# Kernel tuning notes

Hardware: AMD Instinct MI355X
Metric: run time of the kernel (lower is better)

Reference implementation:

```python
import jax, jax.numpy as jnp
import numpy as np

B, SP, SS = 8, 512, 64          # batch, prefix seq len, suffix seq len
HP, HS = 2048, 1024             # prefix / suffix hidden sizes
NH, NKV, HD = 8, 1, 256         # heads, kv heads, head dim (GQA groups = 8)
IP, IS = 16384, 4096            # MLP intermediate sizes
COND = 1024                     # adaRMSNorm conditioning dim
T = SP + SS
EPS = 1e-6
SCALE = HD ** -0.5
ROPE_BASE = 10000.0


def _rms(x):
    var = jnp.mean(jnp.square(x), axis=-1, keepdims=True)
    return x * jax.lax.rsqrt(var + EPS)


def _rot_half(x):
    x1, x2 = jnp.split(x, 2, axis=-1)
    return jnp.concatenate([-x2, x1], axis=-1)


def setup_inputs() -> dict:
    key = jax.random.key(0)
    ks = iter(jax.random.split(key, 40))
    rn = lambda shape, s=0.02: jax.random.normal(next(ks), shape, dtype=jnp.float32) * s
    return dict(
        x_prefix=rn((B, SP, HP), 1.0),
        x_suffix=rn((B, SS, HS), 1.0),
        cond=rn((B, COND), 1.0),
        attention_mask=jnp.zeros((B, 1, T, T), jnp.float32),
        p_ln1_w=rn((HP,)),
        p_q=rn((NH * HD, HP)), p_k=rn((NKV * HD, HP)), p_v=rn((NKV * HD, HP)), p_o=rn((HP, NH * HD)),
        p_ln2_w=rn((HP,)),
        p_gate=rn((IP, HP)), p_up=rn((IP, HP)), p_down=rn((HP, IP)),
        s_ada1_w=rn((3 * HS, COND)), s_ada1_b=rn((3 * HS,)),
        s_q=rn((NH * HD, HS)), s_k=rn((NKV * HD, HS)), s_v=rn((NKV * HD, HS)), s_o=rn((HS, NH * HD)),
        s_ada2_w=rn((3 * HS, COND)), s_ada2_b=rn((3 * HS,)),
        s_gate=rn((IS, HS)), s_up=rn((IS, HS)), s_down=rn((HS, IS)),
        position_ids=jnp.broadcast_to(jnp.arange(T, dtype=jnp.int32), (B, T)),
    )


def _ada_norm(x, cond, w, b):
    # AdaRMSNormV2: rms(x)*(1+scale)+shift; gate returned separately
    mod = cond @ w.T + b                      # [B, 3*HS]
    scale, shift, gate = jnp.split(mod, 3, axis=-1)
    normed = _rms(x) * (1.0 + scale[:, None, :]) + shift[:, None, :]
    return normed, gate[:, None, :]


def _qkv(h, wq, wk, wv):
    b, t, _ = h.shape
    q = (h @ wq.T).reshape(b, t, NH, HD).transpose(0, 2, 1, 3)   # [B,NH,t,HD]
    k = (h @ wk.T).reshape(b, t, NKV, HD).transpose(0, 2, 1, 3)  # [B,1,t,HD]
    v = (h @ wv.T).reshape(b, t, NKV, HD).transpose(0, 2, 1, 3)
    return q, k, v


def reference(x_prefix, x_suffix, cond, attention_mask,
              p_ln1_w, p_q, p_k, p_v, p_o, p_ln2_w, p_gate, p_up, p_down,
              s_ada1_w, s_ada1_b, s_q, s_k, s_v, s_o, s_ada2_w, s_ada2_b,
              s_gate, s_up, s_down, position_ids):
    # --- pre-attention norms ---
    hp = _rms(x_prefix) * (1.0 + p_ln1_w)                  # plain RMSNorm, gate=None
    hs, gate1 = _ada_norm(x_suffix, cond, s_ada1_w, s_ada1_b)

    qp, kp, vp = _qkv(hp, p_q, p_k, p_v)
    qs, ks, vs = _qkv(hs, s_q, s_k, s_v)
    q = jnp.concatenate([qp, qs], axis=2)                  # [B,NH,T,HD]
    k = jnp.concatenate([kp, ks], axis=2)                  # [B,1,T,HD]
    v = jnp.concatenate([vp, vs], axis=2)

    # --- RoPE over joint sequence ---
    inv_freq = 1.0 / (ROPE_BASE ** (jnp.arange(0, HD, 2, dtype=jnp.float32) / HD))
    freqs = position_ids.astype(jnp.float32)[:, :, None] * inv_freq  # [B,T,HD/2]
    emb = jnp.concatenate([freqs, freqs], axis=-1)
    cos = jnp.cos(emb)[:, None]                            # [B,1,T,HD]
    sin = jnp.sin(emb)[:, None]
    q = q * cos + _rot_half(q) * sin
    k = k * cos + _rot_half(k) * sin

    # --- joint attention (GQA: single kv head broadcast over NH query heads) ---
    k0, v0 = k[:, 0], v[:, 0]                              # [B,T,HD]
    scores = jnp.einsum('bhqd,bkd->bhqk', q, k0) * SCALE
    scores = scores + attention_mask
    probs = jax.nn.softmax(scores, axis=-1)
    attn = jnp.einsum('bhqk,bkd->bhqd', probs, v0)
    attn = attn.transpose(0, 2, 1, 3).reshape(B, T, NH * HD)

    a_p, a_s = attn[:, :SP], attn[:, SP:]

    # --- prefix stream: o_proj + residual + RMSNorm + GeGLU MLP ---
    res_p = x_prefix + a_p @ p_o.T
    h = _rms(res_p) * (1.0 + p_ln2_w)
    mlp_p = (jax.nn.gelu(h @ p_gate.T, approximate=True) * (h @ p_up.T)) @ p_down.T
    out_prefix = res_p + mlp_p

    # --- suffix stream: gated residual + adaRMSNorm + GeGLU MLP + gated residual ---
    res_s = x_suffix + (a_s @ s_o.T) * gate1
    h2, gate2 = _ada_norm(res_s, cond, s_ada2_w, s_ada2_b)
    mlp_s = (jax.nn.gelu(h2 @ s_gate.T, approximate=True) * (h2 @ s_up.T)) @ s_down.T
    out_suffix = res_s + mlp_s * gate2

    return (out_prefix, out_suffix)
```

## Files before the change

### kernel.cpp

```cpp
#include <hip/hip_runtime.h>
#include <cstdint>
#include <cstddef>

typedef __bf16 bf;
typedef __attribute__((ext_vector_type(8))) __bf16 bf16x8;
typedef __attribute__((ext_vector_type(4))) float f32x4;
typedef long long ll;

#define DEV __device__ __forceinline__

constexpr int Tt = 576;
constexpr int NHh = 8;
constexpr float EPSf = 1e-6f;
constexpr float SCALEf = 0.0625f;
constexpr float LN1E4_OVER_128 = 0.07195578515606394f;

constexpr int EPI_F32 = 0, EPI_SCALE_BF16 = 1, EPI_BF16 = 2, EPI_GELU_BF16 = 3,
              EPI_MUL_BF16 = 4, EPI_RES_F32 = 5, EPI_RESGATE_F32 = 6;

DEV float wsum(float v) {
#pragma unroll
  for (int o = 32; o > 0; o >>= 1) v += __shfl_xor(v, o, 64);
  return v;
}
DEV float wmaxr(float v) {
#pragma unroll
  for (int o = 32; o > 0; o >>= 1) v = fmaxf(v, __shfl_xor(v, o, 64));
  return v;
}
DEV float gelu_tanh(float x) {
  float x3 = x * x * x;
  float t = tanhf(0.7978845608028654f * (x + 0.044715f * x3));
  return 0.5f * x * (1.0f + t);
}

DEV void gld16(const void* g, void* l) {
  __builtin_amdgcn_global_load_lds(
      (__attribute__((address_space(1))) void*)(g),
      (__attribute__((address_space(3))) void*)(l), 16, 0, 0);
}


__global__ void f2b_k(const float* __restrict__ s, bf* __restrict__ d, int n8) {
  int i = blockIdx.x * 256 + threadIdx.x;
  int stride = gridDim.x * 256;
  for (; i < n8; i += stride) {
    f32x4 a = ((const f32x4*)s)[i * 2];
    f32x4 b = ((const f32x4*)s)[i * 2 + 1];
    bf16x8 w;
    w[0] = (bf)a[0]; w[1] = (bf)a[1]; w[2] = (bf)a[2]; w[3] = (bf)a[3];
    w[4] = (bf)b[0]; w[5] = (bf)b[1]; w[6] = (bf)b[2]; w[7] = (bf)b[3];
    ((bf16x8*)d)[i] = w;
  }
}

__global__ void rms_scale_2048(const float* __restrict__ x, const float* __restrict__ w,
                               bf* __restrict__ out) {
  int row = blockIdx.x;
  int tid = threadIdx.x;
  const float* xr = x + (ll)row * 2048;
  f32x4 a = *(const f32x4*)(xr + tid * 4);
  f32x4 b = *(const f32x4*)(xr + 1024 + tid * 4);
  float ss = a[0]*a[0]+a[1]*a[1]+a[2]*a[2]+a[3]*a[3]
           + b[0]*b[0]+b[1]*b[1]+b[2]*b[2]+b[3]*b[3];
  ss = wsum(ss);
  __shared__ float red[4];
  if ((tid & 63) == 0) red[tid >> 6] = ss;
  __syncthreads();
  float tot = red[0] + red[1] + red[2] + red[3];
  float sc = rsqrtf(tot * (1.0f / 2048.0f) + EPSf);
  bf* o = out + (ll)row * 2048;
#pragma unroll
  for (int j = 0; j < 4; j++) {
    int c0 = tid * 4 + j;
    o[c0]        = (bf)(a[j] * sc * (1.0f + w[c0]));
    o[1024 + c0] = (bf)(b[j] * sc * (1.0f + w[1024 + c0]));
  }
}

__global__ void ada_mod_k(const float* __restrict__ cond, const float* __restrict__ w,
                          const float* __restrict__ bias, float* __restrict__ mod) {
  int n = blockIdx.x * 256 + threadIdx.x;
  int b = blockIdx.y;
  const float* c = cond + b * 1024;
  const float* wr = w + (ll)n * 1024;
  float s = 0.f;
  for (int k = 0; k < 1024; k += 4) {
    f32x4 cv = *(const f32x4*)(c + k);
    f32x4 wv = *(const f32x4*)(wr + k);
    s += cv[0]*wv[0] + cv[1]*wv[1] + cv[2]*wv[2] + cv[3]*wv[3];
  }
  mod[b * 3072 + n] = s + bias[n];
}

__global__ void ada_norm_k(const float* __restrict__ x, const float* __restrict__ mod,
                           bf* __restrict__ out) {
  int row = blockIdx.x;
  int b = row >> 6;
  int tid = threadIdx.x;
  const float* xr = x + (ll)row * 1024;
  f32x4 a = *(const f32x4*)(xr + tid * 4);
  float ss = a[0]*a[0] + a[1]*a[1] + a[2]*a[2] + a[3]*a[3];
  ss = wsum(ss);
  __shared__ float red[4];
  if ((tid & 63) == 0) red[tid >> 6] = ss;
  __syncthreads();
  float tot = red[0] + red[1] + red[2] + red[3];
  float sc = rsqrtf(tot * (1.0f / 1024.0f) + EPSf);
  const float* m = mod + b * 3072;
  bf* o = out + (ll)row * 1024;
#pragma unroll
  for (int j = 0; j < 4; j++) {
    int c = tid * 4 + j;
    o[c] = (bf)(a[j] * sc * (1.0f + m[c]) + m[1024 + c]);
  }
}

__global__ void rope_k(const float* __restrict__ qkv,
                       const int* __restrict__ pos, bf* __restrict__ qb,
                       bf* __restrict__ kb, bf* __restrict__ vT) {
  int bt = blockIdx.x;
  int b = bt / Tt, t = bt - b * Tt;
  int tid = threadIdx.x;
  float p = (float)pos[bt];
  const float* qr = qkv + (ll)bt * 2560;
#pragma unroll
  for (int j = 0; j < 4; j++) {
    int pi = tid + 256 * j;
    int h = pi >> 7, d = pi & 127;
    float ang = p * expf((float)d * (-LN1E4_OVER_128));
    float sn = sinf(ang), cs = cosf(ang);
    float x1 = qr[h * 256 + d], x2 = qr[h * 256 + d + 128];
    bf* qo = qb + ((ll)(b * NHh + h) * Tt + t) * 256;
    qo[d]       = (bf)(x1 * cs - x2 * sn);
    qo[d + 128] = (bf)(x2 * cs + x1 * sn);
  }
  const float* kvr = qr + 2048;
  if (tid < 128) {
    int d = tid;
    float ang = p * expf((float)d * (-LN1E4_OVER_128));
    float sn = sinf(ang), cs = cosf(ang);
    float x1 = kvr[d], x2 = kvr[d + 128];
    bf* ko = kb + (ll)bt * 256;
    ko[d]       = (bf)(x1 * cs - x2 * sn);
    ko[d + 128] = (bf)(x2 * cs + x1 * sn);
  } else {
    int d = tid - 128;
    const float* vv = kvr + 256;
    vT[((ll)b * 256 + d) * Tt + t]       = (bf)vv[d];
    vT[((ll)b * 256 + d + 128) * Tt + t] = (bf)vv[d + 128];
  }
}

__global__ void softmax_k(const bf* __restrict__ scores, const float* __restrict__ mask,
                          bf* __restrict__ probs) {
  int rowg = blockIdx.x * 4 + (threadIdx.x >> 6);
  int lane = threadIdx.x & 63;
  int z = rowg / Tt;
  int t = rowg - z * Tt;
  int b = z >> 3;
  const bf* s = scores + (ll)rowg * Tt;
  const float* mr = mask + ((ll)b * Tt + t) * Tt;
  float v[9];
#pragma unroll
  for (int j = 0; j < 9; j++) {
    int c = lane + j * 64;
    v[j] = (float)s[c] + mr[c];
  }
  float mx = v[0];
#pragma unroll
  for (int j = 1; j < 9; j++) mx = fmaxf(mx, v[j]);
  mx = wmaxr(mx);
  float sum = 0.f;
#pragma unroll
  for (int j = 0; j < 9; j++) { v[j] = __expf(v[j] - mx); sum += v[j]; }
  sum = wsum(sum);
  float inv = 1.0f / sum;
  bf* pr = probs + (ll)rowg * Tt;
#pragma unroll
  for (int j = 0; j < 9; j++) pr[lane + j * 64] = (bf)(v[j] * inv);
}


struct GemmArgs {
  const bf* A; ll sA; int lda;
  const void* Bp; ll sB; int ldb; int zdivB;
  void* C; ll sC; ll sC2; int zdivC; int ldc;
  int M, N, K;
  const float* res; ll sRes;
  const float* gate; ll sGate;
  const bf* aux; ll sAux;
  float alpha;
};

template <int EPI>
DEV void epilogue(const GemmArgs& g, f32x4 (&acc)[4][4], int z, int m0, int n0,
                  int lane, int wr, int wc) {
  const ll coff = (ll)(z / g.zdivC) * g.sC + (ll)(z % g.zdivC) * g.sC2;
  const int r0 = (lane >> 4) * 4;
  const int cc = lane & 15;
#pragma unroll
  for (int m = 0; m < 4; m++) {
#pragma unroll
    for (int n = 0; n < 4; n++) {
      int col = n0 + wc * 64 + n * 16 + cc;
      if (col >= g.N) continue;
#pragma unroll
      for (int r = 0; r < 4; r++) {
        int row = m0 + wr * 64 + m * 16 + r0 + r;
        if (row >= g.M) continue;
        float v = acc[m][n][r];
        ll idx = (ll)row * g.ldc + col;
        if constexpr (EPI == EPI_F32) {
          ((float*)g.C)[coff + idx] = v;
        } else if constexpr (EPI == EPI_SCALE_BF16) {
          ((bf*)g.C)[coff + idx] = (bf)(v * g.alpha);
        } else if constexpr (EPI == EPI_BF16) {
          ((bf*)g.C)[coff + idx] = (bf)v;
        } else if constexpr (EPI == EPI_GELU_BF16) {
          ((bf*)g.C)[coff + idx] = (bf)gelu_tanh(v);
        } else if constexpr (EPI == EPI_MUL_BF16) {
          float a0 = (float)g.aux[(ll)z * g.sAux + idx];
          ((bf*)g.C)[coff + idx] = (bf)(a0 * v);
        } else if constexpr (EPI == EPI_RES_F32) {
          ((float*)g.C)[coff + idx] = g.res[(ll)z * g.sRes + idx] + v;
        } else if constexpr (EPI == EPI_RESGATE_F32) {
          ((float*)g.C)[coff + idx] =
              g.res[(ll)z * g.sRes + idx] + v * g.gate[(ll)z * g.sGate + col];
        }
      }
    }
  }
}

template <int EPI, int BN>
__global__ __launch_bounds__(512) void gemm_8p(GemmArgs g) {
  constexpr int NF = BN / 64;
  constexpr int WN = BN / 4;
  const int z = blockIdx.z;
  const int m0 = blockIdx.x * 256;
  const int n0 = blockIdx.y * BN;
  const int tid = threadIdx.x;
  const int lane = tid & 63;
  const int wv = tid >> 6;
  const int wr = wv >> 2;
  const int wc = wv & 3;

  const bf* A = g.A + (ll)z * g.sA;
  const bf* B = (const bf*)g.Bp + (ll)(z / g.zdivB) * g.sB;

  __shared__ __align__(16) bf lA[2][256 * 64];
  __shared__ __align__(16) bf lB[2][BN * 64];

  f32x4 acc[8][NF];
  f32x4 zero = {0.f, 0.f, 0.f, 0.f};
#pragma unroll
  for (int m = 0; m < 8; m++)
#pragma unroll
    for (int n = 0; n < NF; n++) acc[m][n] = zero;

  const int lrow = lane >> 3;
  const int lsrc = ((lane & 7) ^ lrow) * 8;

  auto stage128 = [&](const bf* src, int ld, int grow0, bf* lds) {
#pragma unroll
    for (int i = 0; i < 2; i++) {
      int chunk = wv * 2 + i;
      gld16(src + (ll)(grow0 + chunk * 8 + lrow) * ld + lsrc, lds + chunk * 512);
    }
  };

  const int NT = g.K >> 6;
  stage128(B, g.ldb, n0, &lB[0][0]);
  if (BN == 256) stage128(B, g.ldb, n0 + 128, &lB[0][128 * 64]);
  stage128(A, g.lda, m0, &lA[0][0]);
  stage128(A, g.lda, m0 + 128, &lA[0][128 * 64]);
  asm volatile("s_waitcnt vmcnt(0)" ::: "memory");
  __builtin_amdgcn_s_barrier();

  for (int t = 0; t < NT; ++t) {
    const int c = t & 1;
    const int nx = (t + 1 < NT) ? t + 1 : t;
    const ll kkn = (ll)nx * 64;
    bf16x8 bv[NF][2];
#pragma unroll
    for (int p = 0; p < 4; ++p) {
      if (p == 0) {
#pragma unroll
        for (int n = 0; n < NF; ++n)
#pragma unroll
          for (int kb = 0; kb < 2; ++kb) {
            int row = wc * WN + n * 16 + (lane & 15);
            int ko = kb * 32 + (lane >> 4) * 8;
            bv[n][kb] = *(const bf16x8*)&lB[c][row * 64 + (ko ^ ((row & 7) * 8))];
          }
      }
      bf16x8 af[2][2];
#pragma unroll
      for (int ml = 0; ml < 2; ++ml)
#pragma unroll
        for (int kb = 0; kb < 2; ++kb) {
          int row = wr * 128 + (2 * p + ml) * 16 + (lane & 15);
          int ko = kb * 32 + (lane >> 4) * 8;
          af[ml][kb] = *(const bf16x8*)&lA[c][row * 64 + (ko ^ ((row & 7) * 8))];
        }
      if (p == 0) {
        stage128(B + kkn, g.ldb, n0, &lB[1 - c][0]);
        if (BN == 256) stage128(B + kkn, g.ldb, n0 + 128, &lB[1 - c][128 * 64]);
      } else if (p == 1) {
        stage128(A + kkn, g.lda, m0, &lA[1 - c][0]);
        stage128(A + kkn, g.lda, m0 + 128, &lA[1 - c][128 * 64]);
      }
      __builtin_amdgcn_s_barrier();
      asm volatile("s_waitcnt lgkmcnt(0)" ::: "memory");
      __builtin_amdgcn_s_setprio(1);
#pragma unroll
      for (int kb = 0; kb < 2; ++kb)
#pragma unroll
        for (int ml = 0; ml < 2; ++ml)
#pragma unroll
          for (int n = 0; n < NF; ++n)
            acc[2 * p + ml][n] = __builtin_amdgcn_mfma_f32_16x16x32_bf16(
                af[ml][kb], bv[n][kb], acc[2 * p + ml][n], 0, 0, 0);
      __builtin_amdgcn_s_setprio(0);
      if (p == 3) asm volatile("s_waitcnt vmcnt(0)" ::: "memory");
      __builtin_amdgcn_s_barrier();
    }
  }

  const ll coff = (ll)(z / g.zdivC) * g.sC + (ll)(z % g.zdivC) * g.sC2;
  const int r0 = (lane >> 4) * 4;
  const int cc = lane & 15;
#pragma unroll
  for (int m = 0; m < 8; m++) {
#pragma unroll
    for (int n = 0; n < NF; n++) {
      int col = n0 + wc * WN + n * 16 + cc;
#pragma unroll
      for (int r = 0; r < 4; r++) {
        int row = m0 + wr * 128 + m * 16 + r0 + r;
        float v = acc[m][n][r];
        ll idx = (ll)row * g.ldc + col;
        if constexpr (EPI == EPI_F32) {
          ((float*)g.C)[coff + idx] = v;
        } else if constexpr (EPI == EPI_GELU_BF16) {
          ((bf*)g.C)[coff + idx] = (bf)gelu_tanh(v);
        } else if constexpr (EPI == EPI_MUL_BF16) {
          float a0 = (float)g.aux[(ll)z * g.sAux + idx];
          ((bf*)g.C)[coff + idx] = (bf)(a0 * v);
        } else if constexpr (EPI == EPI_RES_F32) {
          ((float*)g.C)[coff + idx] = g.res[(ll)z * g.sRes + idx] + v;
        }
      }
    }
  }
}

struct FusedArgs {
  const bf* A; int lda;
  const bf* B1; const bf* B2; int ldb;
  bf* C; int ldc;
  int K;
};

__global__ __launch_bounds__(512) void gemm_8pf(FusedArgs g) {
  const int m0 = blockIdx.x * 256;
  const int n0 = blockIdx.y * 128;
  const int tid = threadIdx.x;
  const int lane = tid & 63;
  const int wv = tid >> 6;
  const int wr = wv >> 2;
  const int wc = wv & 3;

  __shared__ __align__(16) bf lA[2][256 * 64];
  __shared__ __align__(16) bf lB1[2][128 * 64];
  __shared__ __align__(16) bf lB2[2][128 * 64];

  f32x4 acc1[8][2], acc2[8][2];
  f32x4 zero = {0.f, 0.f, 0.f, 0.f};
#pragma unroll
  for (int m = 0; m < 8; m++)
#pragma unroll
    for (int n = 0; n < 2; n++) { acc1[m][n] = zero; acc2[m][n] = zero; }

  const int lrow = lane >> 3;
  const int lsrc = ((lane & 7) ^ lrow) * 8;

  auto stage128 = [&](const bf* src, int ld, int grow0, bf* lds) {
#pragma unroll
    for (int i = 0; i < 2; i++) {
      int chunk = wv * 2 + i;
      gld16(src + (ll)(grow0 + chunk * 8 + lrow) * ld + lsrc, lds + chunk * 512);
    }
  };

  const int NT = g.K >> 6;
  stage128(g.B1, g.ldb, n0, &lB1[0][0]);
  stage128(g.B2, g.ldb, n0, &lB2[0][0]);
  stage128(g.A, g.lda, m0, &lA[0][0]);
  stage128(g.A, g.lda, m0 + 128, &lA[0][128 * 64]);
  asm volatile("s_waitcnt vmcnt(0)" ::: "memory");
  __builtin_amdgcn_s_barrier();

  for (int t = 0; t < NT; ++t) {
    const int c = t & 1;
    const int nx = (t + 1 < NT) ? t + 1 : t;
    const ll kkn = (ll)nx * 64;
    bf16x8 b1v[2][2], b2v[2][2];
#pragma unroll
    for (int p = 0; p < 4; ++p) {
      if (p == 0) {
#pragma unroll
        for (int n = 0; n < 2; ++n)
#pragma unroll
          for (int kb = 0; kb < 2; ++kb) {
            int row = wc * 32 + n * 16 + (lane & 15);
            int ko = kb * 32 + (lane >> 4) * 8;
            int sw = row * 64 + (ko ^ ((row & 7) * 8));
            b1v[n][kb] = *(const bf16x8*)&lB1[c][sw];
            b2v[n][kb] = *(const bf16x8*)&lB2[c][sw];
          }
      }
      bf16x8 af[2][2];
#pragma unroll
      for (int ml = 0; ml < 2; ++ml)
#pragma unroll
        for (int kb = 0; kb < 2; ++kb) {
          int row = wr * 128 + (2 * p + ml) * 16 + (lane & 15);
          int ko = kb * 32 + (lane >> 4) * 8;
          af[ml][kb] = *(const bf16x8*)&lA[c][row * 64 + (ko ^ ((row & 7) * 8))];
        }
      if (p == 0) {
        stage128(g.B1 + kkn, g.ldb, n0, &lB1[1 - c][0]);
        stage128(g.B2 + kkn, g.ldb, n0, &lB2[1 - c][0]);
      } else if (p == 1) {
        stage128(g.A + kkn, g.lda, m0, &lA[1 - c][0]);
        stage128(g.A + kkn, g.lda, m0 + 128, &lA[1 - c][128 * 64]);
      }
      __builtin_amdgcn_s_barrier();
      asm volatile("s_waitcnt lgkmcnt(0)" ::: "memory");
      __builtin_amdgcn_s_setprio(1);
#pragma unroll
      for (int kb = 0; kb < 2; ++kb)
#pragma unroll
        for (int ml = 0; ml < 2; ++ml)
#pragma unroll
          for (int n = 0; n < 2; ++n) {
            acc1[2 * p + ml][n] = __builtin_amdgcn_mfma_f32_16x16x32_bf16(
                af[ml][kb], b1v[n][kb], acc1[2 * p + ml][n], 0, 0, 0);
            acc2[2 * p + ml][n] = __builtin_amdgcn_mfma_f32_16x16x32_bf16(
                af[ml][kb], b2v[n][kb], acc2[2 * p + ml][n], 0, 0, 0);
          }
      __builtin_amdgcn_s_setprio(0);
      if (p == 3) asm volatile("s_waitcnt vmcnt(0)" ::: "memory");
      __builtin_amdgcn_s_barrier();
    }
  }

  const int r0 = (lane >> 4) * 4;
  const int cc = lane & 15;
#pragma unroll
  for (int m = 0; m < 8; m++) {
#pragma unroll
    for (int n = 0; n < 2; n++) {
      int col = n0 + wc * 32 + n * 16 + cc;
#pragma unroll
      for (int r = 0; r < 4; r++) {
        int row = m0 + wr * 128 + m * 16 + r0 + r;
        g.C[(ll)row * g.ldc + col] =
            (bf)(gelu_tanh(acc1[m][n][r]) * acc2[m][n][r]);
      }
    }
  }
}

template <int EPI>
__global__ __launch_bounds__(256) void gemm_p(GemmArgs g) {
  const int z = blockIdx.z;
  const int m0 = blockIdx.x * 128;
  const int n0 = blockIdx.y * 128;
  const int tid = threadIdx.x;
  const int lane = tid & 63;
  const int wid = tid >> 6;
  const int wr = wid >> 1, wc = wid & 1;

  const bf* A = g.A + (ll)z * g.sA;
  const bf* B = (const bf*)g.Bp + (ll)(z / g.zdivB) * g.sB;

  __shared__ __align__(16) bf lA[2][128 * 64];
  __shared__ __align__(16) bf lB[2][128 * 64];

  f32x4 acc[4][4];
  f32x4 zero = {0.f, 0.f, 0.f, 0.f};
#pragma unroll
  for (int m = 0; m < 4; m++)
#pragma unroll
    for (int n = 0; n < 4; n++) acc[m][n] = zero;

  const int lrow = lane >> 3;
  const int lsrc = ((lane & 7) ^ lrow) * 8;

  auto stage = [&](int kt, int bsel) {
    const ll kk = (ll)kt * 64;
#pragma unroll
    for (int i = 0; i < 4; i++) {
      int rr = wid * 32 + i * 8;
      int ra = m0 + rr + lrow; if (ra > g.M - 1) ra = g.M - 1;
      gld16(A + (ll)ra * g.lda + kk + lsrc, &lA[bsel][rr * 64]);
      int rb = n0 + rr + lrow; if (rb > g.N - 1) rb = g.N - 1;
      gld16(B + (ll)rb * g.ldb + kk + lsrc, &lB[bsel][rr * 64]);
    }
  };

  const int nt = g.K >> 6;
  stage(0, 0);
  stage(nt > 1 ? 1 : 0, 1);

  for (int t = 0; t < nt; ++t) {
    const int cur = t & 1;
    asm volatile("s_waitcnt vmcnt(8)" ::: "memory");
    __builtin_amdgcn_s_barrier();
    asm volatile("" ::: "memory");
#pragma unroll
    for (int kb = 0; kb < 2; kb++) {
      const int ko = kb * 32 + (lane >> 4) * 8;
      bf16x8 af[4], bv[4];
#pragma unroll
      for (int m = 0; m < 4; m++) {
        int row = wr * 64 + m * 16 + (lane & 15);
        af[m] = *(const bf16x8*)&lA[cur][row * 64 + (ko ^ ((row & 7) * 8))];
      }
#pragma unroll
      for (int n = 0; n < 4; n++) {
        int row = wc * 64 + n * 16 + (lane & 15);
        bv[n] = *(const bf16x8*)&lB[cur][row * 64 + (ko ^ ((row & 7) * 8))];
      }
      __builtin_amdgcn_s_setprio(1);
#pragma unroll
      for (int m = 0; m < 4; m++)
#pragma unroll
        for (int n = 0; n < 4; n++)
          acc[m][n] = __builtin_amdgcn_mfma_f32_16x16x32_bf16(af[m], bv[n], acc[m][n], 0, 0, 0);
      __builtin_amdgcn_s_setprio(0);
    }
    asm volatile("" ::: "memory");
    __builtin_amdgcn_s_barrier();
    asm volatile("" ::: "memory");
    int nxt = t + 2; if (nxt > nt - 1) nxt = nt - 1;
    stage(nxt, cur);
  }
  epilogue<EPI>(g, acc, z, m0, n0, lane, wr, wc);
}

template <int EPI>
__global__ __launch_bounds__(256) void gemm_rs(GemmArgs g) {
  const int z = blockIdx.z;
  const int m0 = blockIdx.x * 128;
  const int n0 = blockIdx.y * 128;
  const int tid = threadIdx.x;
  const int lane = tid & 63;
  const int wid = tid >> 6;
  const int wr = wid >> 1, wc = wid & 1;

  const bf* A = g.A + (ll)z * g.sA;
  const float* Bf = (const float*)g.Bp + (ll)(z / g.zdivB) * g.sB;

  __shared__ __align__(16) bf lA[128 * 64];
  __shared__ __align__(16) bf lB[128 * 64];

  f32x4 acc[4][4];
  f32x4 zero = {0.f, 0.f, 0.f, 0.f};
#pragma unroll
  for (int m = 0; m < 4; m++)
#pragma unroll
    for (int n = 0; n < 4; n++) acc[m][n] = zero;

  const int srow = tid >> 3;
  const int scol = (tid & 7) * 8;

  for (int kk = 0; kk < g.K; kk += 64) {
#pragma unroll
    for (int i = 0; i < 4; i++) {
      int r = m0 + i * 32 + srow;
      if (r > g.M - 1) r = g.M - 1;
      f32x4 v = *(const f32x4*)(A + (ll)r * g.lda + kk + scol);
      *(f32x4*)&lA[(i * 32 + srow) * 64 + scol] = v;
    }
#pragma unroll
    for (int i = 0; i < 4; i++) {
      int r = n0 + i * 32 + srow;
      if (r > g.N - 1) r = g.N - 1;
      const float* src = Bf + (ll)r * g.ldb + kk + scol;
      f32x4 v0 = *(const f32x4*)(src);
      f32x4 v1 = *(const f32x4*)(src + 4);
      bf16x8 w;
      w[0] = (bf)v0[0]; w[1] = (bf)v0[1]; w[2] = (bf)v0[2]; w[3] = (bf)v0[3];
      w[4] = (bf)v1[0]; w[5] = (bf)v1[1]; w[6] = (bf)v1[2]; w[7] = (bf)v1[3];
      *(bf16x8*)&lB[(i * 32 + srow) * 64 + scol] = w;
    }
    __syncthreads();
#pragma unroll
    for (int kb = 0; kb < 2; kb++) {
      const int ko = kb * 32 + (lane >> 4) * 8;
      bf16x8 af[4], bfv[4];
#pragma unroll
      for (int m = 0; m < 4; m++)
        af[m] = *(const bf16x8*)&lA[(wr * 64 + m * 16 + (lane & 15)) * 64 + ko];
#pragma unroll
      for (int n = 0; n < 4; n++)
        bfv[n] = *(const bf16x8*)&lB[(wc * 64 + n * 16 + (lane & 15)) * 64 + ko];
#pragma unroll
      for (int m = 0; m < 4; m++)
#pragma unroll
        for (int n = 0; n < 4; n++)
          acc[m][n] = __builtin_amdgcn_mfma_f32_16x16x32_bf16(af[m], bfv[n], acc[m][n], 0, 0, 0);
    }
    __syncthreads();
  }
  epilogue<EPI>(g, acc, z, m0, n0, lane, wr, wc);
}


static GemmArgs mkG(const bf* A, ll sA, int lda, const void* Bp, ll sB, int ldb, int zdivB,
                    void* C, ll sC, ll sC2, int zdivC, int ldc, int M, int N, int K) {
  GemmArgs g{};
  g.A = A; g.sA = sA; g.lda = lda;
  g.Bp = Bp; g.sB = sB; g.ldb = ldb; g.zdivB = zdivB;
  g.C = C; g.sC = sC; g.sC2 = sC2; g.zdivC = zdivC; g.ldc = ldc;
  g.M = M; g.N = N; g.K = K;
  g.res = nullptr; g.sRes = 0; g.gate = nullptr; g.sGate = 0; g.aux = nullptr; g.sAux = 0;
  g.alpha = 1.0f;
  return g;
}

extern "C" void kernel_launch(void* const* d_in, const int* in_sizes, int n_in,
                              void* d_out, int out_size, void* d_ws, size_t ws_size,
                              hipStream_t stream) {
  (void)in_sizes; (void)n_in; (void)out_size;
  const float* x_prefix = (const float*)d_in[0];
  const float* x_suffix = (const float*)d_in[1];
  const float* cond     = (const float*)d_in[2];
  const float* mask     = (const float*)d_in[3];
  const float* p_ln1_w  = (const float*)d_in[4];
  const float* p_q      = (const float*)d_in[5];
  const float* p_k      = (const float*)d_in[6];
  const float* p_v      = (const float*)d_in[7];
  const float* p_o      = (const float*)d_in[8];
  const float* p_ln2_w  = (const float*)d_in[9];
  const float* p_gate   = (const float*)d_in[10];
  const float* p_up     = (const float*)d_in[11];
  const float* p_down   = (const float*)d_in[12];
  const float* s_ada1_w = (const float*)d_in[13];
  const float* s_ada1_b = (const float*)d_in[14];
  const float* s_q      = (const float*)d_in[15];
  const float* s_k      = (const float*)d_in[16];
  const float* s_v      = (const float*)d_in[17];
  const float* s_o      = (const float*)d_in[18];
  const float* s_ada2_w = (const float*)d_in[19];
  const float* s_ada2_b = (const float*)d_in[20];
  const float* s_gate   = (const float*)d_in[21];
  const float* s_up     = (const float*)d_in[22];
  const float* s_down   = (const float*)d_in[23];
  const int*   pos      = (const int*)d_in[24];

  char* base = (char*)d_ws;
  size_t off = 0;
  auto alloc = [&](size_t bytes) {
    char* p = base + off;
    off = (off + bytes + 255) & ~(size_t)255;
    return p;
  };
  float* qkv   = (float*)alloc(8ll * Tt * 2560 * 4);
  bf* hp     = (bf*)alloc(4096ll * 2048 * 2);
  bf* hs     = (bf*)alloc(512ll * 1024 * 2);
  float* mod1 = (float*)alloc(8 * 3072 * 4);
  float* mod2 = (float*)alloc(8 * 3072 * 4);
  bf* qb     = (bf*)alloc(64ll * Tt * 256 * 2);
  bf* kb     = (bf*)alloc(8ll * Tt * 256 * 2);
  bf* vT     = (bf*)alloc(8ll * 256 * Tt * 2);
  bf* scores = (bf*)alloc(64ll * Tt * Tt * 2);
  float* res_p = (float*)alloc(8ll * 512 * 2048 * 4);
  float* res_s = (float*)alloc(8ll * 64 * 1024 * 4);
  bf* gbuf   = (bf*)alloc(4096ll * 16384 * 2);

  bf* attn   = (bf*)qkv;
  bf* hbuf   = hp;
  bf* h2     = hs;
  bf* probs  = scores;
  bf* gbuf_s = gbuf;

  struct WEnt { const float* src; bf* dst; ll n; };
  WEnt went[14] = {
    {p_q,    nullptr, 2048ll * 2048}, {p_k,    nullptr, 256ll * 2048},
    {p_v,    nullptr, 256ll * 2048},  {p_o,    nullptr, 2048ll * 2048},
    {p_gate, nullptr, 16384ll * 2048},{p_up,   nullptr, 16384ll * 2048},
    {p_down, nullptr, 2048ll * 16384},{s_q,    nullptr, 2048ll * 1024},
    {s_k,    nullptr, 256ll * 1024},  {s_v,    nullptr, 256ll * 1024},
    {s_o,    nullptr, 1024ll * 2048}, {s_gate, nullptr, 4096ll * 1024},
    {s_up,   nullptr, 4096ll * 1024}, {s_down, nullptr, 1024ll * 4096},
  };
  for (int i = 0; i < 14; i++) went[i].dst = (bf*)alloc((size_t)went[i].n * 2);
  const bool conv = (off <= ws_size);

  float* outp = (float*)d_out;
  float* outs = outp + 8ll * 512 * 2048;

  dim3 blk(256);

  if (conv) {
    for (int i = 0; i < 14; i++) {
      int n8 = (int)(went[i].n / 8);
      int grid = (n8 + 255) / 256; if (grid > 4096) grid = 4096;
      f2b_k<<<grid, 256, 0, stream>>>(went[i].src, went[i].dst, n8);
    }
  }
  const bf* w_pqkv = went[0].dst;
  const bf* w_po = went[3].dst, *w_pg = went[4].dst, *w_pu = went[5].dst,
          *w_pd = went[6].dst;
  const bf* w_sqkv = went[7].dst;
  const bf* w_so = went[10].dst, *w_sg = went[11].dst,
          *w_su = went[12].dst, *w_sd = went[13].dst;

  auto launchW = [&](int epi, GemmArgs g, const float* wf32, const bf* wbf,
                     dim3 grid) {
    if (conv) {
      g.Bp = wbf;
      switch (epi) {
        case EPI_F32:        gemm_p<EPI_F32><<<grid, blk, 0, stream>>>(g); break;
        case EPI_GELU_BF16:  gemm_p<EPI_GELU_BF16><<<grid, blk, 0, stream>>>(g); break;
        case EPI_MUL_BF16:   gemm_p<EPI_MUL_BF16><<<grid, blk, 0, stream>>>(g); break;
        case EPI_RES_F32:    gemm_p<EPI_RES_F32><<<grid, blk, 0, stream>>>(g); break;
        case EPI_RESGATE_F32:gemm_p<EPI_RESGATE_F32><<<grid, blk, 0, stream>>>(g); break;
      }
    } else {
      g.Bp = wf32;
      switch (epi) {
        case EPI_F32:        gemm_rs<EPI_F32><<<grid, blk, 0, stream>>>(g); break;
        case EPI_GELU_BF16:  gemm_rs<EPI_GELU_BF16><<<grid, blk, 0, stream>>>(g); break;
        case EPI_MUL_BF16:   gemm_rs<EPI_MUL_BF16><<<grid, blk, 0, stream>>>(g); break;
        case EPI_RES_F32:    gemm_rs<EPI_RES_F32><<<grid, blk, 0, stream>>>(g); break;
        case EPI_RESGATE_F32:gemm_rs<EPI_RESGATE_F32><<<grid, blk, 0, stream>>>(g); break;
      }
    }
  };

  rms_scale_2048<<<4096, 256, 0, stream>>>(x_prefix, p_ln1_w, hp);
  ada_mod_k<<<dim3(12, 8), 256, 0, stream>>>(cond, s_ada1_w, s_ada1_b, mod1);
  ada_norm_k<<<512, 256, 0, stream>>>(x_suffix, mod1, hs);

  if (conv) {
    GemmArgs g = mkG(hp, 512ll * 2048, 2048, w_pqkv, 0, 2048, 1,
                     qkv, (ll)Tt * 2560, 0, 1, 2560, 512, 2560, 2048);
    gemm_8p<EPI_F32, 128><<<dim3(2, 20, 8), 512, 0, stream>>>(g);
  } else {
    launchW(EPI_F32, mkG(hp, 512ll * 2048, 2048, nullptr, 0, 2048, 1,
                         qkv, (ll)Tt * 2560, 0, 1, 2560, 512, 2048, 2048),
            p_q, nullptr, dim3(4, 16, 8));
    launchW(EPI_F32, mkG(hp, 512ll * 2048, 2048, nullptr, 0, 2048, 1,
                         qkv + 2048, (ll)Tt * 2560, 0, 1, 2560, 512, 256, 2048),
            p_k, nullptr, dim3(4, 2, 8));
    launchW(EPI_F32, mkG(hp, 512ll * 2048, 2048, nullptr, 0, 2048, 1,
                         qkv + 2304, (ll)Tt * 2560, 0, 1, 2560, 512, 256, 2048),
            p_v, nullptr, dim3(4, 2, 8));
  }
  if (conv) {
    GemmArgs g = mkG(hs, 64ll * 1024, 1024, w_sqkv, 0, 1024, 1,
                     qkv + 512ll * 2560, (ll)Tt * 2560, 0, 1, 2560, 64, 2560, 1024);
    gemm_p<EPI_F32><<<dim3(1, 20, 8), blk, 0, stream>>>(g);
  } else {
    launchW(EPI_F32, mkG(hs, 64ll * 1024, 1024, nullptr, 0, 1024, 1,
                         qkv + 512ll * 2560, (ll)Tt * 2560, 0, 1, 2560, 64, 2048, 1024),
            s_q, nullptr, dim3(1, 16, 8));
    launchW(EPI_F32, mkG(hs, 64ll * 1024, 1024, nullptr, 0, 1024, 1,
                         qkv + 512ll * 2560 + 2048, (ll)Tt * 2560, 0, 1, 2560, 64, 256, 1024),
            s_k, nullptr, dim3(1, 2, 8));
    launchW(EPI_F32, mkG(hs, 64ll * 1024, 1024, nullptr, 0, 1024, 1,
                         qkv + 512ll * 2560 + 2304, (ll)Tt * 2560, 0, 1, 2560, 64, 256, 1024),
            s_v, nullptr, dim3(1, 2, 8));
  }
  rope_k<<<8 * Tt, 256, 0, stream>>>(qkv, pos, qb, kb, vT);

  {
    GemmArgs g = mkG(qb, (ll)Tt * 256, 256, kb, (ll)Tt * 256, 256, 8,
                     scores, (ll)Tt * Tt, 0, 1, Tt, Tt, Tt, 256);
    g.alpha = SCALEf;
    gemm_p<EPI_SCALE_BF16><<<dim3(5, 5, 64), blk, 0, stream>>>(g);
  }
  softmax_k<<<64 * Tt / 4, 256, 0, stream>>>(scores, mask, probs);
  {
    GemmArgs g = mkG(probs, (ll)Tt * Tt, Tt, vT, 256ll * Tt, Tt, 8,
                     attn, (ll)Tt * 2048, 256, 8, 2048, Tt, 256, Tt);
    gemm_p<EPI_BF16><<<dim3(5, 2, 64), blk, 0, stream>>>(g);
  }
  {
    GemmArgs g = mkG(attn, (ll)Tt * 2048, 2048, w_po, 0, 2048, 1,
                     res_p, 512ll * 2048, 0, 1, 2048, 512, 2048, 2048);
    g.res = x_prefix; g.sRes = 512ll * 2048;
    if (conv) gemm_8p<EPI_RES_F32, 128><<<dim3(2, 16, 8), 512, 0, stream>>>(g);
    else      launchW(EPI_RES_F32, g, p_o, w_po, dim3(4, 16, 8));
  }
  {
    GemmArgs g = mkG(attn + 512ll * 2048, (ll)Tt * 2048, 2048, nullptr, 0, 2048, 1,
                     res_s, 64ll * 1024, 0, 1, 1024, 64, 1024, 2048);
    g.res = x_suffix; g.sRes = 64ll * 1024;
    g.gate = mod1 + 2048; g.sGate = 3072;
    launchW(EPI_RESGATE_F32, g, s_o, w_so, dim3(1, 8, 8));
  }
  rms_scale_2048<<<4096, 256, 0, stream>>>(res_p, p_ln2_w, hbuf);
  ada_mod_k<<<dim3(12, 8), 256, 0, stream>>>(cond, s_ada2_w, s_ada2_b, mod2);
  ada_norm_k<<<512, 256, 0, stream>>>(res_s, mod2, h2);

  if (conv) {
    FusedArgs fg{hbuf, 2048, w_pg, w_pu, 2048, gbuf, 16384, 2048};
    gemm_8pf<<<dim3(16, 128, 1), 512, 0, stream>>>(fg);
  } else {
    launchW(EPI_GELU_BF16, mkG(hbuf, 0, 2048, nullptr, 0, 2048, 1,
                               gbuf, 0, 0, 1, 16384, 4096, 16384, 2048),
            p_gate, w_pg, dim3(32, 128, 1));
    GemmArgs g = mkG(hbuf, 0, 2048, nullptr, 0, 2048, 1,
                     gbuf, 0, 0, 1, 16384, 4096, 16384, 2048);
    g.aux = gbuf; g.sAux = 0;
    launchW(EPI_MUL_BF16, g, p_up, w_pu, dim3(32, 128, 1));
  }
  {
    GemmArgs g = mkG(gbuf, 0, 16384, w_pd, 0, 16384, 1,
                     outp, 0, 0, 1, 2048, 4096, 2048, 16384);
    g.res = res_p; g.sRes = 0;
    if (conv) gemm_8p<EPI_RES_F32, 128><<<dim3(16, 16, 1), 512, 0, stream>>>(g);
    else      launchW(EPI_RES_F32, g, p_down, w_pd, dim3(32, 16, 1));
  }
  if (conv) {
    FusedArgs fg{h2, 1024, w_sg, w_su, 1024, gbuf_s, 4096, 1024};
    gemm_8pf<<<dim3(2, 32, 1), 512, 0, stream>>>(fg);
  } else {
    launchW(EPI_GELU_BF16, mkG(h2, 0, 1024, nullptr, 0, 1024, 1,
                               gbuf_s, 0, 0, 1, 4096, 512, 4096, 1024),
            s_gate, w_sg, dim3(4, 32, 1));
    GemmArgs g = mkG(h2, 0, 1024, nullptr, 0, 1024, 1,
                     gbuf_s, 0, 0, 1, 4096, 512, 4096, 1024);
    g.aux = gbuf_s; g.sAux = 0;
    launchW(EPI_MUL_BF16, g, s_up, w_su, dim3(4, 32, 1));
  }
  {
    GemmArgs g = mkG(gbuf_s, 64ll * 4096, 4096, nullptr, 0, 4096, 1,
                     outs, 64ll * 1024, 0, 1, 1024, 64, 1024, 4096);
    g.res = res_s; g.sRes = 64ll * 1024;
    g.gate = mod2 + 2048; g.sGate = 3072;
    launchW(EPI_RESGATE_F32, g, s_down, w_sd, dim3(1, 8, 8));
  }
}
```

Measured before the change: 1.831 ms.

## Merge weight conversions into one launch and swizzle GEMM block order

Replaces the fourteen separate fp32-to-bf16 weight conversion launches with a single grid-stride kernel that finds the source tensor through a cumulative offset table. It relies on the destination buffers being laid out contiguously. Both big GEMM kernels also remap block indices with a stride-8 swizzle so that blocks running at the same time touch different tiles, meant to spread work across XCDs/L2 for better cache locality. The swizzle assumes the grid size is divisible by 8, otherwise some tiles may be skipped.

```diff
diff --git a/kernel.cpp b/kernel.cpp
--- a/kernel.cpp
+++ b/kernel.cpp
@@ -41,16 +41,26 @@
 }
 
 
-__global__ void f2b_k(const float* __restrict__ s, bf* __restrict__ d, int n8) {
+struct CvtArgs {
+  const float* src[14];
+  ll cum8[15];
+  bf* dst;
+};
+
+__global__ void f2b_all(CvtArgs a, int totN8) {
   int i = blockIdx.x * 256 + threadIdx.x;
   int stride = gridDim.x * 256;
-  for (; i < n8; i += stride) {
-    f32x4 a = ((const f32x4*)s)[i * 2];
-    f32x4 b = ((const f32x4*)s)[i * 2 + 1];
+  for (; i < totN8; i += stride) {
+    int s = 0;
+#pragma unroll
+    for (int j = 1; j < 14; j++) if (i >= a.cum8[j]) s = j;
+    const float* sp = a.src[s] + ((ll)i - a.cum8[s]) * 8;
+    f32x4 v0 = *(const f32x4*)sp;
+    f32x4 v1 = *(const f32x4*)(sp + 4);
     bf16x8 w;
-    w[0] = (bf)a[0]; w[1] = (bf)a[1]; w[2] = (bf)a[2]; w[3] = (bf)a[3];
-    w[4] = (bf)b[0]; w[5] = (bf)b[1]; w[6] = (bf)b[2]; w[7] = (bf)b[3];
-    ((bf16x8*)d)[i] = w;
+    w[0] = (bf)v0[0]; w[1] = (bf)v0[1]; w[2] = (bf)v0[2]; w[3] = (bf)v0[3];
+    w[4] = (bf)v1[0]; w[5] = (bf)v1[1]; w[6] = (bf)v1[2]; w[7] = (bf)v1[3];
+    ((bf16x8*)a.dst)[i] = w;
   }
 }
 
@@ -238,8 +248,12 @@
   constexpr int NF = BN / 64;
   constexpr int WN = BN / 4;
   const int z = blockIdx.z;
-  const int m0 = blockIdx.x * 256;
-  const int n0 = blockIdx.y * BN;
+  const int nxy = gridDim.x * gridDim.y;
+  const int lin = blockIdx.x + gridDim.x * blockIdx.y;
+  const int q8 = nxy >> 3;
+  const int swz = (lin & 7) * q8 + (lin >> 3);
+  const int m0 = (swz % gridDim.x) * 256;
+  const int n0 = (swz / gridDim.x) * BN;
   const int tid = threadIdx.x;
   const int lane = tid & 63;
   const int wv = tid >> 6;
@@ -364,8 +378,12 @@
 };
 
 __global__ __launch_bounds__(512) void gemm_8pf(FusedArgs g) {
-  const int m0 = blockIdx.x * 256;
-  const int n0 = blockIdx.y * 128;
+  const int nxy = gridDim.x * gridDim.y;
+  const int lin = blockIdx.x + gridDim.x * blockIdx.y;
+  const int q8 = nxy >> 3;
+  const int swz = (lin & 7) * q8 + (lin >> 3);
+  const int m0 = (swz % gridDim.x) * 256;
+  const int n0 = (swz / gridDim.x) * 128;
   const int tid = threadIdx.x;
   const int lane = tid & 63;
   const int wv = tid >> 6;
@@ -708,11 +726,12 @@
   dim3 blk(256);
 
   if (conv) {
-    for (int i = 0; i < 14; i++) {
-      int n8 = (int)(went[i].n / 8);
-      int grid = (n8 + 255) / 256; if (grid > 4096) grid = 4096;
-      f2b_k<<<grid, 256, 0, stream>>>(went[i].src, went[i].dst, n8);
-    }
+    CvtArgs ca{};
+    ll c = 0;
+    for (int i = 0; i < 14; i++) { ca.src[i] = went[i].src; ca.cum8[i] = c; c += went[i].n / 8; }
+    ca.cum8[14] = c;
+    ca.dst = went[0].dst;
+    f2b_all<<<2048, 256, 0, stream>>>(ca, (int)c);
   }
   const bf* w_pqkv = went[0].dst;
   const bf* w_po = went[3].dst, *w_pg = went[4].dst, *w_pu = went[5].dst,
```

After: 1.953 ms. 6.7% more time.
